# Optimization experiments

Hardware: AMD Instinct MI355X
Metric: run time of the kernel (lower is better)

## Reference

```python
import jax, jax.numpy as jnp
import numpy as np

N = 1024
H = 4096
W = 4096
K_COUNTS = 10
IOU_T = 0.5
NEG = -1e30  # -inf stand-in for unrecorded groups


def _box_iou(b):
    # b: [N,4] xyxy pixel coords -> [N,N] IoU (torchvision.ops.box_iou)
    area = (b[:, 2] - b[:, 0]) * (b[:, 3] - b[:, 1])
    ix1 = jnp.maximum(b[:, None, 0], b[None, :, 0])
    iy1 = jnp.maximum(b[:, None, 1], b[None, :, 1])
    ix2 = jnp.minimum(b[:, None, 2], b[None, :, 2])
    iy2 = jnp.minimum(b[:, None, 3], b[None, :, 3])
    inter = jnp.clip(ix2 - ix1, 0.0) * jnp.clip(iy2 - iy1, 0.0)
    return inter / (area[:, None] + area[None, :] - inter)


def _c_wsl(iou_gt, scores, counts):
    # Faithful vectorized c_wsl_fast: for every start box i, greedily sweep
    # j = i+1..N-1 adding boxes compatible (IoU <= T) with all current members;
    # when a group hits `counts` at the TOP of a j-iteration it is recorded
    # (check-before-add semantics, so a group completed at j = N-1 is never
    # recorded, matching the original break-based control flow). The final
    # answer is the LAST start achieving the max recorded score (>= update).
    n = scores.shape[0]
    starts = jnp.arange(n)
    carry0 = (
        jnp.eye(n, dtype=bool),            # sel[i, k]: box k in group of start i
        jnp.ones(n, jnp.int32),            # group sizes
        scores,                            # group scores
        jnp.zeros(n, bool),                # recorded flag (== break)
        jnp.full(n, NEG, scores.dtype),    # recorded score
        jnp.zeros((n, n), bool),           # recorded membership
    )

    def step(c, xs):
        j, sj, iou_j = xs  # iou_j = iou_gt[j] (> T bool row; matrix symmetric)
        sel, size, score, rec, rec_score, rec_sel = c
        active = (j > starts) & (~rec)
        do_rec = active & (size == counts)
        rec_sel = jnp.where(do_rec[:, None], sel, rec_sel)
        rec_score = jnp.where(do_rec, score, rec_score)
        rec = rec | do_rec
        compat = ~jnp.any(sel & iou_j[None, :], axis=1)
        add = active & (~do_rec) & (size < counts) & compat
        sel = sel.at[:, j].set(sel[:, j] | add)
        size = size + add.astype(size.dtype)
        score = score + jnp.where(add, sj, jnp.zeros((), score.dtype))
        return (sel, size, score, rec, rec_score, rec_sel), None

    (_, _, _, rec, rec_score, rec_sel), _ = jax.lax.scan(
        step, carry0, (starts, scores, iou_gt))
    masked = jnp.where(rec, rec_score, NEG)
    best = (n - 1) - jnp.argmax(masked[::-1])  # last argmax == '>=' update rule
    return jnp.where(jnp.any(rec), rec_sel[best], jnp.zeros(n, bool))


def reference(bbox, obj_scores, probs, counts):
    Hh, Ww = probs.shape
    # score_bbox_heatmap(reduction='mean'): mean of probs[y1:y2, x1:x2] per box,
    # computed exactly for all boxes with a zero-padded summed-area table.
    sat = jnp.pad(jnp.cumsum(jnp.cumsum(probs, axis=0), axis=1), ((1, 0), (1, 0)))
    x1 = jnp.clip(jnp.floor(bbox[:, 0]).astype(jnp.int32), 0, Ww)
    y1 = jnp.clip(jnp.floor(bbox[:, 1]).astype(jnp.int32), 0, Hh)
    x2 = jnp.clip(jnp.floor(bbox[:, 2]).astype(jnp.int32), 0, Ww)
    y2 = jnp.clip(jnp.floor(bbox[:, 3]).astype(jnp.int32), 0, Hh)
    sums = sat[y2, x2] - sat[y1, x2] - sat[y2, x1] + sat[y1, x1]
    cnt = jnp.maximum((y2 - y1) * (x2 - x1), 1).astype(probs.dtype)
    box_scores = sums / cnt
    # agg_score_method == 'mean'
    scores = 0.5 * (obj_scores + box_scores)
    # sort descending, then greedy IoU grouping on sorted boxes
    order = jnp.argsort(-scores)
    bbox_s = bbox[order]
    scores_s = scores[order]
    iou_gt = _box_iou(bbox_s) > IOU_T
    sel = _c_wsl(iou_gt, scores_s, counts)
    return scores_s * sel.astype(scores_s.dtype)


def setup_inputs() -> dict:
    key = jax.random.key(0)
    k1, k2, k3, k4, k5, k6 = jax.random.split(key, 6)
    cx = jax.random.uniform(k1, (N,), minval=0.15, maxval=0.85) * W
    cy = jax.random.uniform(k2, (N,), minval=0.15, maxval=0.85) * H
    bw = jnp.maximum(jax.random.uniform(k3, (N,), minval=0.02, maxval=0.25) * W, 8.0)
    bh = jnp.maximum(jax.random.uniform(k4, (N,), minval=0.02, maxval=0.25) * H, 8.0)
    bbox = jnp.stack([cx - bw / 2, cy - bh / 2, cx + bw / 2, cy + bh / 2], axis=1)
    obj_scores = jax.random.uniform(k5, (N,))
    probs = jax.random.uniform(k6, (H, W))
    return {"bbox": bbox, "obj_scores": obj_scores, "probs": probs, "counts": K_COUNTS}
```

## Files before the change

### kernel.cpp

```cpp
#include <hip/hip_runtime.h>

#define HH 4096
#define WW 4096
#define NB 1024
#define NCHUNK 256
#define CROWS 16
#define NSEG 16
#define IOU_T 0.5f
#define NBLK_STAGE 1024
#define NBLK_TAIL 256

typedef unsigned long long u64;

constexpr size_t OFF_PART   = 0;
constexpr size_t OFF_SC64   = OFF_PART   + (size_t)NCHUNK * WW * 8;
constexpr size_t OFF_ORDER  = OFF_SC64   + (size_t)NB * 8;
constexpr size_t OFF_CTR    = OFF_ORDER  + (size_t)NB * 4;
constexpr size_t OFF_IOU    = OFF_CTR    + 64;
constexpr size_t OFF_RECSC  = OFF_IOU    + (size_t)NB * 16 * 8;
constexpr size_t OFF_RECSEL = OFF_RECSC  + (size_t)NB * 8;
constexpr size_t OFF_CC     = OFF_RECSEL + (size_t)NB * 16 * 8;
constexpr size_t OFF_SEG    = OFF_CC     + (size_t)HH * WW * 4;
constexpr size_t OFF_PART2  = OFF_SEG    + (size_t)NSEG * WW * 8;

template <typename T>
__device__ __forceinline__ void st_c(T* p, T v) {
    __hip_atomic_store(p, v, __ATOMIC_RELAXED, __HIP_MEMORY_SCOPE_AGENT);
}

__device__ __forceinline__ void gbar(int* bctr, int round) {
    asm volatile("s_waitcnt vmcnt(0)" ::: "memory");
    __syncthreads();
    if (threadIdx.x == 0) {
        __hip_atomic_fetch_add(bctr, 1, __ATOMIC_RELAXED, __HIP_MEMORY_SCOPE_AGENT);
        while (__hip_atomic_load(bctr, __ATOMIC_RELAXED, __HIP_MEMORY_SCOPE_AGENT)
               < NBLK_TAIL * round)
            __builtin_amdgcn_s_sleep(2);
    }
    __syncthreads();
}


__global__ void __launch_bounds__(256) k_stage(const float* __restrict__ probs,
        const float* __restrict__ bbox,
        double* __restrict__ part, float* __restrict__ Cc, int* __restrict__ ctrs) {
    __shared__ int xlo_s[CROWS], xhi_s[CROWS];
    __shared__ int2 rng_s[CROWS];
    int tid = blockIdx.x * 256 + threadIdx.x;
    int c  = tid >> 10;
    int xq = tid & 1023;
    int t  = threadIdx.x;
    if (blockIdx.x == 0 && t == 0) st_c(&ctrs[1], 0);
    if (t < CROWS) { xlo_s[t] = WW + 1; xhi_s[t] = -1; }
    __syncthreads();
    int r0 = c * CROWS;
    for (int i = t; i < NB; i += 256) {
        float4 bb = ((const float4*)bbox)[i];
        int x1 = min(max((int)floorf(bb.x), 0), WW);
        int y1 = min(max((int)floorf(bb.y), 0), HH);
        int x2 = min(max((int)floorf(bb.z), 0), WW);
        int y2 = min(max((int)floorf(bb.w), 0), HH);
        int ra = y1 - 1 - r0, rb = y2 - 1 - r0;
        if (ra >= 0 && ra < CROWS) { atomicMin(&xlo_s[ra], x1); atomicMax(&xhi_s[ra], x2); }
        if (rb >= 0 && rb < CROWS) { atomicMin(&xlo_s[rb], x1); atomicMax(&xhi_s[rb], x2); }
    }
    __syncthreads();
    if (t < CROWS) {
        int lo = xlo_s[t], hi = xhi_s[t];
        rng_s[t] = (hi >= 0) ? make_int2(lo >> 2, (hi + 3) >> 2) : make_int2(1, 0);
    }
    __syncthreads();
    const float4* p = (const float4*)probs + (size_t)r0 * (WW / 4) + xq;
    float4* Cc4 = (float4*)Cc;
    double a0 = 0.0, a1 = 0.0, a2 = 0.0, a3 = 0.0;
    for (int r = 0; r < CROWS; r += 8) {
        float4 q[8];
        #pragma unroll
        for (int k = 0; k < 8; k++) q[k] = p[(size_t)(r + k) * (WW / 4)];
        #pragma unroll
        for (int k = 0; k < 8; k++) {
            a0 += (double)q[k].x; a1 += (double)q[k].y;
            a2 += (double)q[k].z; a3 += (double)q[k].w;
            int2 d = rng_s[r + k];
            if (xq >= d.x && xq < d.y)
                Cc4[(size_t)(r0 + r + k) * (WW / 4) + xq] =
                    make_float4((float)a0, (float)a1, (float)a2, (float)a3);
        }
    }
    double2* pp = (double2*)(part + (size_t)c * WW) + xq * 2;
    pp[0] = make_double2(a0, a1);
    pp[1] = make_double2(a2, a3);
}

__global__ void __launch_bounds__(1024) k_tail(const float* __restrict__ bbox,
        const float* __restrict__ obj,
        const float* __restrict__ Cc,
        const double* __restrict__ part,
        double* __restrict__ segsum, double* __restrict__ part2,
        const int* __restrict__ counts,
        double* __restrict__ sc64, int* __restrict__ order,
        u64* __restrict__ ioub, double* __restrict__ recsc,
        u64* __restrict__ recsel, int* __restrict__ ctrs,
        float* __restrict__ out) {
    __shared__ double s_sc[NB];
    __shared__ int    ord_s[NB];
    __shared__ alignas(16) u64 big[NB * 16];
    __shared__ double red[16];
    __shared__ int    redi[16];
    float4* sbb = (float4*)big;
    int b = blockIdx.x, t = threadIdx.x;
    int gtid = b * 1024 + t;
    int* bctr = &ctrs[1];

    if (b < 64) {
        int col = gtid & (WW - 1);
        int seg = gtid >> 12;
        const double* pp = part + (size_t)seg * CROWS * WW + col;
        double s = 0.0;
        #pragma unroll
        for (int k = 0; k < 16; k++) s += pp[(size_t)k * WW];
        st_c(&segsum[(size_t)seg * WW + col], s);
    }
    gbar(bctr, 1);

    if (b < 64) {
        int col = gtid & (WW - 1);
        int seg = gtid >> 12;
        double carry = 0.0;
        for (int s = 0; s < seg; s++) carry += segsum[(size_t)s * WW + col];
        const double* pp = part  + (size_t)seg * CROWS * WW + col;
        double*       qq = part2 + (size_t)seg * CROWS * WW + col;
        #pragma unroll
        for (int k = 0; k < 16; k++) {
            double v = pp[(size_t)k * WW];
            st_c(&qq[(size_t)k * WW], carry);
            carry += v;
        }
    }
    gbar(bctr, 2);

    {
        int bg = t >> 8;
        int tl = t & 255;
        int i = b * 4 + bg;
        float4 bb = ((const float4*)bbox)[i];
        int x1 = min(max((int)floorf(bb.x), 0), WW);
        int y1 = min(max((int)floorf(bb.y), 0), HH);
        int x2 = min(max((int)floorf(bb.z), 0), WW);
        int y2 = min(max((int)floorf(bb.w), 0), HH);
        bool h1 = (y1 >= 1), h2 = (y2 >= 1);
        const float*  r2 = Cc    + (size_t)(h2 ? (y2 - 1) : 0) * WW;
        const double* q2 = part2 + (size_t)(h2 ? ((y2 - 1) >> 4) : 0) * WW;
        const float*  r1 = Cc    + (size_t)(h1 ? (y1 - 1) : 0) * WW;
        const double* q1 = part2 + (size_t)(h1 ? ((y1 - 1) >> 4) : 0) * WW;
        double s = 0.0;
        for (int x = x1 + tl; x < x2; x += 256) {
            double v2 = h2 ? ((double)r2[x] + q2[x]) : 0.0;
            double v1 = h1 ? ((double)r1[x] + q1[x]) : 0.0;
            s += (v2 - v1);
        }
        #pragma unroll
        for (int off = 32; off > 0; off >>= 1) s += __shfl_down(s, off);
        if ((t & 63) == 0) red[t >> 6] = s;
        __syncthreads();
        if (tl == 0) {
            double tot = red[bg * 4] + red[bg * 4 + 1] + red[bg * 4 + 2] + red[bg * 4 + 3];
            long long cnt = (long long)(y2 - y1) * (long long)(x2 - x1);
            if (cnt < 1) cnt = 1;
            st_c(&sc64[i], 0.5 * ((double)obj[i] + tot / (double)cnt));
        }
    }
    gbar(bctr, 3);

    s_sc[t] = sc64[t];
    __syncthreads();
    {
        int bg = t >> 8;
        int tl = t & 255;
        int i = b * 4 + bg;
        double si = s_sc[i];
        int p = 0;
        #pragma unroll
        for (int it = 0; it < 4; it++) {
            int j = tl * 4 + it;
            double sj = s_sc[j];
            p += (sj > si) || (sj == si && j < i);
        }
        #pragma unroll
        for (int off = 32; off > 0; off >>= 1) p += __shfl_down(p, off);
        if ((t & 63) == 0) redi[t >> 6] = p;
        __syncthreads();
        if (t < 4) {
            int r = redi[t * 4] + redi[t * 4 + 1] + redi[t * 4 + 2] + redi[t * 4 + 3];
            st_c(&order[r], b * 4 + t);
        }
    }
    gbar(bctr, 4);

    {
        int o = order[t];
        ord_s[t] = o;
        sbb[t] = ((const float4*)bbox)[o];
    }
    __syncthreads();
    {
        int l = t & 63;
        for (int task = t >> 6; task < 64; task += 16) {
            int r = task >> 4, wd = task & 15;
            int i = b * 4 + r;
            float4 a = sbb[i];
            float ai = (a.z - a.x) * (a.w - a.y);
            float4 bb = sbb[(wd << 6) + l];
            float aj = (bb.z - bb.x) * (bb.w - bb.y);
            float ix1 = fmaxf(a.x, bb.x), iy1 = fmaxf(a.y, bb.y);
            float ix2 = fminf(a.z, bb.z), iy2 = fminf(a.w, bb.w);
            float iw = fmaxf(ix2 - ix1, 0.0f), ih = fmaxf(iy2 - iy1, 0.0f);
            float inter = iw * ih;
            float iou_v = inter / (ai + aj - inter);
            u64 m = __ballot(iou_v > IOU_T);
            if (l == 0) st_c(&ioub[(size_t)i * 16 + wd], m);
        }
    }
    gbar(bctr, 5);

    #pragma unroll
    for (int k = 0; k < 16; k++) big[t + k * 1024] = ioub[t + k * 1024];
    __syncthreads();
    {
        int K = counts[0];
        if (t < 4) {
            int i = b * 4 + t;
            u64 inc[16], sel[16];
            int wi = i >> 6, bi = i & 63;
            #pragma unroll
            for (int w = 0; w < 16; w++) {
                inc[w] = big[i * 16 + w];
                sel[w] = (w == wi) ? (1ULL << bi) : 0ULL;
            }
            int size = 1;
            double score = s_sc[ord_s[i]];
            int last = i;
            #pragma unroll
            for (int w = 0; w < 16; w++) {
                if (w < wi || size >= K) continue;
                u64 avail = ~inc[w];
                if (w == wi) avail &= (bi == 63) ? 0ULL : (~0ULL << (bi + 1));
                while (avail != 0ULL && size < K) {
                    int bj = __builtin_ctzll(avail);
                    int j = (w << 6) + bj;
                    sel[w] |= 1ULL << bj;
                    size++;
                    score += s_sc[ord_s[j]];
                    last = j;
                    const u64* rj = &big[j * 16];
                    #pragma unroll
                    for (int w2 = 0; w2 < 16; w2++) inc[w2] |= rj[w2];
                    avail &= ~inc[w];
                    avail &= ~(1ULL << bj);
                }
            }
            int rec = (size == K) && (last < NB - 1);
            st_c(&recsc[i], rec ? score : -1e300);
            #pragma unroll
            for (int w = 0; w < 16; w++) st_c(&recsel[(size_t)i * 16 + w], sel[w]);
        }
    }
    gbar(bctr, 6);
    if (b != 0) return;

    if (t < 64) {
        double bs = -1e301; int bidx = 0;
        for (int m = 0; m < 16; m++) {
            int k = t * 16 + m;
            double v = recsc[k];
            if (v >= bs) { bs = v; bidx = k; }
        }
        #pragma unroll
        for (int off = 32; off > 0; off >>= 1) {
            double ob = __shfl_down(bs, off);
            int oi = __shfl_down(bidx, off);
            if (ob > bs || (ob == bs && oi > bidx)) { bs = ob; bidx = oi; }
        }
        bs = __shfl(bs, 0);
        bidx = __shfl(bidx, 0);
        int any = bs > -1e299;
        for (int k = t; k < NB; k += 64) {
            float v = 0.0f;
            if (any && ((recsel[(size_t)bidx * 16 + (k >> 6)] >> (k & 63)) & 1ULL))
                v = (float)s_sc[ord_s[k]];
            out[k] = v;
        }
    }
}


extern "C" void kernel_launch(void* const* d_in, const int* in_sizes, int n_in,
                              void* d_out, int out_size, void* d_ws, size_t ws_size,
                              hipStream_t stream) {
    const float* bbox  = (const float*)d_in[0];
    const float* obj   = (const float*)d_in[1];
    const float* probs = (const float*)d_in[2];
    const int*   counts = (const int*)d_in[3];
    float* out = (float*)d_out;

    char* w = (char*)d_ws;
    double* part    = (double*)(w + OFF_PART);
    double* sc64    = (double*)(w + OFF_SC64);
    int*    order   = (int*)(w + OFF_ORDER);
    int*    ctrs    = (int*)(w + OFF_CTR);
    u64*    ioub    = (u64*)(w + OFF_IOU);
    double* recsc   = (double*)(w + OFF_RECSC);
    u64*    recsel  = (u64*)(w + OFF_RECSEL);
    float*  Cc      = (float*)(w + OFF_CC);
    double* segsum  = (double*)(w + OFF_SEG);
    double* part2   = (double*)(w + OFF_PART2);

    k_stage<<<NBLK_STAGE, 256, 0, stream>>>(probs, bbox, part, Cc, ctrs);
    k_tail<<<NBLK_TAIL, 1024, 0, stream>>>(bbox, obj, Cc, part, segsum, part2,
                                           counts, sc64, order, ioub, recsc,
                                           recsel, ctrs, out);
}
```

Measured before the change: 162.3 us.

## Move column prefix scan into stage kernel via last-block completion counters

The per-column exclusive prefix scan over chunk partials moves out of the tail kernel, where it took two grid-wide barriers. In k_stage, each block bumps one of 16 sharded counters. The last arriver in each shard spins until all stage blocks finish, then scans a 256-column slice serially over 256 chunks. Counters are now reset with a memset instead of in-kernel, which adds an extra stream operation, and the serial scan by only 16 blocks may sit on the critical path.

Result: slower. 166.5 us (+2.6%).

```diff
diff --git a/kernel.cpp b/kernel.cpp
--- a/kernel.cpp
+++ b/kernel.cpp
@@ -5,7 +5,6 @@
 #define NB 1024
 #define NCHUNK 256
 #define CROWS 16
-#define NSEG 16
 #define IOU_T 0.5f
 #define NBLK_STAGE 1024
 #define NBLK_TAIL 256
@@ -16,12 +15,11 @@
 constexpr size_t OFF_SC64   = OFF_PART   + (size_t)NCHUNK * WW * 8;
 constexpr size_t OFF_ORDER  = OFF_SC64   + (size_t)NB * 8;
 constexpr size_t OFF_CTR    = OFF_ORDER  + (size_t)NB * 4;
-constexpr size_t OFF_IOU    = OFF_CTR    + 64;
+constexpr size_t OFF_IOU    = OFF_CTR    + 4096;
 constexpr size_t OFF_RECSC  = OFF_IOU    + (size_t)NB * 16 * 8;
 constexpr size_t OFF_RECSEL = OFF_RECSC  + (size_t)NB * 8;
 constexpr size_t OFF_CC     = OFF_RECSEL + (size_t)NB * 16 * 8;
-constexpr size_t OFF_SEG    = OFF_CC     + (size_t)HH * WW * 4;
-constexpr size_t OFF_PART2  = OFF_SEG    + (size_t)NSEG * WW * 8;
+constexpr size_t OFF_PART2  = OFF_CC     + (size_t)HH * WW * 4;
 
 template <typename T>
 __device__ __forceinline__ void st_c(T* p, T v) {
@@ -43,14 +41,15 @@
 
 __global__ void __launch_bounds__(256) k_stage(const float* __restrict__ probs,
         const float* __restrict__ bbox,
-        double* __restrict__ part, float* __restrict__ Cc, int* __restrict__ ctrs) {
+        double* __restrict__ part, double* __restrict__ part2,
+        float* __restrict__ Cc, int* __restrict__ ctrs) {
     __shared__ int xlo_s[CROWS], xhi_s[CROWS];
     __shared__ int2 rng_s[CROWS];
+    __shared__ int sIdx;
     int tid = blockIdx.x * 256 + threadIdx.x;
     int c  = tid >> 10;
     int xq = tid & 1023;
     int t  = threadIdx.x;
-    if (blockIdx.x == 0 && t == 0) st_c(&ctrs[1], 0);
     if (t < CROWS) { xlo_s[t] = WW + 1; xhi_s[t] = -1; }
     __syncthreads();
     int r0 = c * CROWS;
@@ -87,16 +86,49 @@
                     make_float4((float)a0, (float)a1, (float)a2, (float)a3);
         }
     }
-    double2* pp = (double2*)(part + (size_t)c * WW) + xq * 2;
-    pp[0] = make_double2(a0, a1);
-    pp[1] = make_double2(a2, a3);
+    size_t pbase = (size_t)c * WW + 4 * (size_t)xq;
+    st_c(&part[pbase + 0], a0);
+    st_c(&part[pbase + 1], a1);
+    st_c(&part[pbase + 2], a2);
+    st_c(&part[pbase + 3], a3);
+
+    asm volatile("s_waitcnt vmcnt(0)" ::: "memory");
+    __syncthreads();
+    if (t == 0)
+        sIdx = __hip_atomic_fetch_add(&ctrs[16 * ((blockIdx.x & 15) + 1)], 1,
+                                      __ATOMIC_RELAXED, __HIP_MEMORY_SCOPE_AGENT);
+    __syncthreads();
+    if (sIdx != 63) return;
+    if (t == 0) {
+        for (;;) {
+            int s = 0;
+            for (int i2 = 0; i2 < 16; i2++)
+                s += __hip_atomic_load(&ctrs[16 * (i2 + 1)], __ATOMIC_RELAXED,
+                                       __HIP_MEMORY_SCOPE_AGENT);
+            if (s == NBLK_STAGE) break;
+            __builtin_amdgcn_s_sleep(2);
+        }
+    }
+    __syncthreads();
+    {
+        int x = (blockIdx.x & 15) * 256 + t;
+        double carry = 0.0;
+        for (int g = 0; g < NCHUNK / 16; g++) {
+            double v[16];
+            #pragma unroll
+            for (int k = 0; k < 16; k++) v[k] = part[(size_t)(g * 16 + k) * WW + x];
+            #pragma unroll
+            for (int k = 0; k < 16; k++) { double tv = v[k]; v[k] = carry; carry += tv; }
+            #pragma unroll
+            for (int k = 0; k < 16; k++) part2[(size_t)(g * 16 + k) * WW + x] = v[k];
+        }
+    }
 }
 
 __global__ void __launch_bounds__(1024) k_tail(const float* __restrict__ bbox,
         const float* __restrict__ obj,
         const float* __restrict__ Cc,
-        const double* __restrict__ part,
-        double* __restrict__ segsum, double* __restrict__ part2,
+        const double* __restrict__ part2,
         const int* __restrict__ counts,
         double* __restrict__ sc64, int* __restrict__ order,
         u64* __restrict__ ioub, double* __restrict__ recsc,
@@ -109,35 +141,7 @@
     __shared__ int    redi[16];
     float4* sbb = (float4*)big;
     int b = blockIdx.x, t = threadIdx.x;
-    int gtid = b * 1024 + t;
-    int* bctr = &ctrs[1];
-
-    if (b < 64) {
-        int col = gtid & (WW - 1);
-        int seg = gtid >> 12;
-        const double* pp = part + (size_t)seg * CROWS * WW + col;
-        double s = 0.0;
-        #pragma unroll
-        for (int k = 0; k < 16; k++) s += pp[(size_t)k * WW];
-        st_c(&segsum[(size_t)seg * WW + col], s);
-    }
-    gbar(bctr, 1);
-
-    if (b < 64) {
-        int col = gtid & (WW - 1);
-        int seg = gtid >> 12;
-        double carry = 0.0;
-        for (int s = 0; s < seg; s++) carry += segsum[(size_t)s * WW + col];
-        const double* pp = part  + (size_t)seg * CROWS * WW + col;
-        double*       qq = part2 + (size_t)seg * CROWS * WW + col;
-        #pragma unroll
-        for (int k = 0; k < 16; k++) {
-            double v = pp[(size_t)k * WW];
-            st_c(&qq[(size_t)k * WW], carry);
-            carry += v;
-        }
-    }
-    gbar(bctr, 2);
+    int* bctr = &ctrs[0];
 
     {
         int bg = t >> 8;
@@ -170,7 +174,7 @@
             st_c(&sc64[i], 0.5 * ((double)obj[i] + tot / (double)cnt));
         }
     }
-    gbar(bctr, 3);
+    gbar(bctr, 1);
 
     s_sc[t] = sc64[t];
     __syncthreads();
@@ -195,7 +199,7 @@
             st_c(&order[r], b * 4 + t);
         }
     }
-    gbar(bctr, 4);
+    gbar(bctr, 2);
 
     {
         int o = order[t];
@@ -221,7 +225,7 @@
             if (l == 0) st_c(&ioub[(size_t)i * 16 + wd], m);
         }
     }
-    gbar(bctr, 5);
+    gbar(bctr, 3);
 
     #pragma unroll
     for (int k = 0; k < 16; k++) big[t + k * 1024] = ioub[t + k * 1024];
@@ -265,7 +269,7 @@
             for (int w = 0; w < 16; w++) st_c(&recsel[(size_t)i * 16 + w], sel[w]);
         }
     }
-    gbar(bctr, 6);
+    gbar(bctr, 4);
     if (b != 0) return;
 
     if (t < 64) {
@@ -312,11 +316,11 @@
     double* recsc   = (double*)(w + OFF_RECSC);
     u64*    recsel  = (u64*)(w + OFF_RECSEL);
     float*  Cc      = (float*)(w + OFF_CC);
-    double* segsum  = (double*)(w + OFF_SEG);
     double* part2   = (double*)(w + OFF_PART2);
 
-    k_stage<<<NBLK_STAGE, 256, 0, stream>>>(probs, bbox, part, Cc, ctrs);
-    k_tail<<<NBLK_TAIL, 1024, 0, stream>>>(bbox, obj, Cc, part, segsum, part2,
-                                           counts, sc64, order, ioub, recsc,
+    hipMemsetAsync(w + OFF_CTR, 0, 4096, stream);
+    k_stage<<<NBLK_STAGE, 256, 0, stream>>>(probs, bbox, part, part2, Cc, ctrs);
+    k_tail<<<NBLK_TAIL, 1024, 0, stream>>>(bbox, obj, Cc, part2, counts,
+                                           sc64, order, ioub, recsc,
                                            recsel, ctrs, out);
 }
```
